# Performance work log

Hardware: AMD Instinct MI355X
Metric: run time of the kernel (lower is better)

Reference implementation:

```python
import jax, jax.numpy as jnp
import numpy as np

N_NODES = 100000
N_EDGES = 1600000
NUM_FEATURES = 128


def setup_inputs() -> dict:
    key = jax.random.key(0)
    ks = jax.random.split(key, 10)
    x = jax.random.normal(ks[0], (N_NODES, NUM_FEATURES), dtype=jnp.float32)
    edge_index = jax.random.randint(ks[1], (2, N_EDGES), 0, N_NODES, dtype=jnp.int64)
    # conv1 MLP: Linear(num_features,128) -> ReLU -> Linear(128,128)
    s1 = 1.0 / np.sqrt(NUM_FEATURES)
    W1 = jax.random.uniform(ks[2], (NUM_FEATURES, 128), jnp.float32, -s1, s1)
    b1 = jax.random.uniform(ks[3], (128,), jnp.float32, -s1, s1)
    s2 = 1.0 / np.sqrt(128)
    W2 = jax.random.uniform(ks[4], (128, 128), jnp.float32, -s2, s2)
    b2 = jax.random.uniform(ks[5], (128,), jnp.float32, -s2, s2)
    # conv2 MLP: Linear(128,64) -> ReLU -> Linear(64,64)
    W3 = jax.random.uniform(ks[6], (128, 64), jnp.float32, -s2, s2)
    b3 = jax.random.uniform(ks[7], (64,), jnp.float32, -s2, s2)
    s3 = 1.0 / np.sqrt(64)
    W4 = jax.random.uniform(ks[8], (64, 64), jnp.float32, -s3, s3)
    b4 = jax.random.uniform(ks[9], (64,), jnp.float32, -s3, s3)
    return {"x": x, "edge_index": edge_index, "W1": W1, "b1": b1,
            "W2": W2, "b2": b2, "W3": W3, "b3": b3, "W4": W4, "b4": b4}


def _gin_conv(x, src, dst, Wa, ba, Wb, bb):
    # GINConv with eps=0: out = MLP(x + sum_{j->i} x_j)
    agg = jax.ops.segment_sum(x[src], dst, num_segments=N_NODES)
    h = x + agg
    h = jax.nn.relu(h @ Wa + ba)
    return h @ Wb + bb


def reference(x, edge_index, W1, b1, W2, b2, W3, b3, W4, b4):
    src, dst = edge_index[0], edge_index[1]
    h = jax.nn.relu(_gin_conv(x, src, dst, W1, b1, W2, b2))
    h = jax.nn.relu(_gin_conv(h, src, dst, W3, b3, W4, b4))
    return h
```

## Files before the change

kernel.cpp:

```cpp
#include <hip/hip_runtime.h>
#include <hip/hip_bf16.h>

#define NODES 100000
#define EDGES 1600000
#define NBINS ((NODES + 127) >> 7)
#define BINCAP 4096
#define PB_BLOCKS 256
#define PB_CHUNK ((EDGES + PB_BLOCKS - 1) / PB_BLOCKS)
#define CAST_BLOCKS 12500
#define WPREP_BLOCKS 176

typedef __bf16 bf16x8 __attribute__((ext_vector_type(8)));
typedef float f32x4 __attribute__((ext_vector_type(4)));

__device__ __forceinline__ unsigned short f2b(float f) {
  __hip_bfloat16 h = __float2bfloat16(f);
  return __builtin_bit_cast(unsigned short, h);
}
__device__ __forceinline__ float b_lo(unsigned u) { return __uint_as_float(u << 16); }
__device__ __forceinline__ float b_hi(unsigned u) { return __uint_as_float(u & 0xffff0000u); }

__global__ __launch_bounds__(256) void prep_count(
    const float4* __restrict__ x4, ushort4* __restrict__ xh4,
    const float* __restrict__ W1, const float* __restrict__ W2,
    const float* __restrict__ W3, const float* __restrict__ W4,
    unsigned short* __restrict__ Wt1, unsigned short* __restrict__ Wt2,
    unsigned short* __restrict__ Wt3, unsigned short* __restrict__ Wt4,
    const int* __restrict__ dst, int* __restrict__ partialT) {
  __shared__ int h[NBINS];
  const int b = blockIdx.x;
  if (b < CAST_BLOCKS) {
    int i = b * 256 + threadIdx.x;
    float4 v = x4[i];
    ushort4 o;
    o.x = f2b(v.x); o.y = f2b(v.y); o.z = f2b(v.z); o.w = f2b(v.w);
    xh4[i] = o;
    return;
  }
  if (b < CAST_BLOCKS + WPREP_BLOCKS) {
    int i = (b - CAST_BLOCKS) * 256 + threadIdx.x;
    if (i < 16384) {
      int n = i >> 7, k = i & 127;
      Wt1[i] = f2b(W1[k * 128 + n]);
    } else if (i < 32768) {
      int j = i - 16384; int n = j >> 7, k = j & 127;
      Wt2[j] = f2b(W2[k * 128 + n]);
    } else if (i < 40960) {
      int j = i - 32768; int n = j >> 7, k = j & 127;
      Wt3[j] = f2b(W3[k * 64 + n]);
    } else if (i < 45056) {
      int j = i - 40960; int n = j >> 6, k = j & 63;
      Wt4[j] = f2b(W4[k * 64 + n]);
    }
    return;
  }
  const int cb = b - CAST_BLOCKS - WPREP_BLOCKS;
  for (int i = threadIdx.x; i < NBINS; i += 256) h[i] = 0;
  __syncthreads();
  const int beg = cb * PB_CHUNK;
  const int end = min(beg + PB_CHUNK, EDGES);
  for (int e = beg + threadIdx.x; e < end; e += 256)
    atomicAdd(&h[dst[e] >> 7], 1);
  __syncthreads();
  for (int i = threadIdx.x; i < NBINS; i += 256)
    partialT[i * PB_BLOCKS + cb] = h[i];
}

__global__ __launch_bounds__(256) void scan_blockoff(const int* __restrict__ partialT,
                                                     int* __restrict__ blockoffT,
                                                     int* __restrict__ binTotal) {
  __shared__ int s[256];
  const int bin = blockIdx.x;
  const int t = threadIdx.x;
  int v = partialT[bin * PB_BLOCKS + t];
  s[t] = v;
  __syncthreads();
  for (int off = 1; off < 256; off <<= 1) {
    int u = (t >= off) ? s[t - off] : 0;
    __syncthreads();
    s[t] += u;
    __syncthreads();
  }
  blockoffT[bin * PB_BLOCKS + t] = s[t] - v;
  if (t == 255) binTotal[bin] = s[255];
}

__global__ __launch_bounds__(1024) void scan_totals(const int* __restrict__ binTotal,
                                                    int* __restrict__ binStart,
                                                    int* __restrict__ rowstart) {
  __shared__ int s[1024];
  const int t = threadIdx.x;
  int v = (t < NBINS) ? binTotal[t] : 0;
  s[t] = v;
  __syncthreads();
  for (int off = 1; off < 1024; off <<= 1) {
    int u = (t >= off) ? s[t - off] : 0;
    __syncthreads();
    s[t] += u;
    __syncthreads();
  }
  if (t < NBINS) binStart[t] = s[t] - v;
  if (t == 0) {
    binStart[NBINS] = EDGES;
    rowstart[NODES] = EDGES;
  }
}

__global__ __launch_bounds__(256) void bin_scatter(const int* __restrict__ src,
                                                   const int* __restrict__ dst,
                                                   const int* __restrict__ binStart,
                                                   const int* __restrict__ blockoffT,
                                                   unsigned* __restrict__ coarse) {
  __shared__ int base[NBINS];
  __shared__ int h[NBINS];
  const int beg = blockIdx.x * PB_CHUNK;
  const int end = min(beg + PB_CHUNK, EDGES);
  for (int i = threadIdx.x; i < NBINS; i += 256) {
    base[i] = binStart[i] + blockoffT[i * PB_BLOCKS + blockIdx.x];
    h[i] = 0;
  }
  __syncthreads();
  for (int e = beg + threadIdx.x; e < end; e += 256) {
    int d = dst[e];
    int b = d >> 7;
    int pos = base[b] + atomicAdd(&h[b], 1);
    coarse[pos] = (unsigned)src[e] | ((unsigned)(d & 127) << 17);
  }
}

__global__ __launch_bounds__(256) void bin_fine(const unsigned* __restrict__ coarse,
                                                const int* __restrict__ binStart,
                                                int* __restrict__ rowstart,
                                                int* __restrict__ bucket) {
  __shared__ unsigned ent[BINCAP];
  __shared__ unsigned obuf[BINCAP];
  __shared__ int deg[128];
  __shared__ int pre[128];
  const int b = blockIdx.x;
  const int t = threadIdx.x;
  const int s0 = binStart[b];
  const int nE = binStart[b + 1] - s0;
  const int binBase = b << 7;

  if (t < 128) deg[t] = 0;
  __syncthreads();
  for (int i = t; i < nE; i += 256) {
    unsigned e = coarse[s0 + i];
    ent[i] = e;
    atomicAdd(&deg[e >> 17], 1);
  }
  __syncthreads();
  int v = 0;
  if (t < 128) {
    v = deg[t];
    pre[t] = v;
  }
  __syncthreads();
  for (int off = 1; off < 128; off <<= 1) {
    int u = (t >= off && t < 128) ? pre[t - off] : 0;
    __syncthreads();
    if (t < 128) pre[t] += u;
    __syncthreads();
  }
  if (t < 128) {
    int ex = pre[t] - v;
    if (binBase + t < NODES) rowstart[binBase + t] = s0 + ex;
    deg[t] = ex;
  }
  __syncthreads();
  for (int i = t; i < nE; i += 256) {
    unsigned e = ent[i];
    int pos = atomicAdd(&deg[e >> 17], 1);
    obuf[pos] = e & 0x1FFFFu;
  }
  __syncthreads();
  for (int i = t; i < nE; i += 256) bucket[s0 + i] = (int)obuf[i];
}

__global__ __launch_bounds__(256) void gather_sum_bf16(
    const uint4* __restrict__ xq, const int* __restrict__ rowstart,
    const int* __restrict__ bucket, uint4* __restrict__ outq) {
  const int n = blockIdx.x * 4 + (threadIdx.x >> 6);
  if (n >= NODES) return;
  const int lane = threadIdx.x & 63;
  const int g = lane >> 4;
  const int fl = lane & 15;

  float a[8] = {0.f, 0.f, 0.f, 0.f, 0.f, 0.f, 0.f, 0.f};
  if (g == 0) {
    uint4 v = xq[(size_t)n * 16 + fl];
    a[0] = b_lo(v.x); a[1] = b_hi(v.x);
    a[2] = b_lo(v.y); a[3] = b_hi(v.y);
    a[4] = b_lo(v.z); a[5] = b_hi(v.z);
    a[6] = b_lo(v.w); a[7] = b_hi(v.w);
  }

  const int beg = rowstart[n];
  const int end = rowstart[n + 1];
  for (int j = beg; j < end; j += 16) {
    int e0 = j + g, e1 = j + 4 + g, e2 = j + 8 + g, e3 = j + 12 + g;
    int i0 = (e0 < end) ? e0 : (end - 1);
    int i1 = (e1 < end) ? e1 : (end - 1);
    int i2 = (e2 < end) ? e2 : (end - 1);
    int i3 = (e3 < end) ? e3 : (end - 1);
    int s0 = bucket[i0], s1 = bucket[i1], s2 = bucket[i2], s3 = bucket[i3];
    uint4 v0 = xq[(size_t)s0 * 16 + fl];
    uint4 v1 = xq[(size_t)s1 * 16 + fl];
    uint4 v2 = xq[(size_t)s2 * 16 + fl];
    uint4 v3 = xq[(size_t)s3 * 16 + fl];
    float m0 = (e0 < end) ? 1.f : 0.f;
    float m1 = (e1 < end) ? 1.f : 0.f;
    float m2 = (e2 < end) ? 1.f : 0.f;
    float m3 = (e3 < end) ? 1.f : 0.f;
    a[0] = fmaf(b_lo(v0.x), m0, a[0]); a[1] = fmaf(b_hi(v0.x), m0, a[1]);
    a[2] = fmaf(b_lo(v0.y), m0, a[2]); a[3] = fmaf(b_hi(v0.y), m0, a[3]);
    a[4] = fmaf(b_lo(v0.z), m0, a[4]); a[5] = fmaf(b_hi(v0.z), m0, a[5]);
    a[6] = fmaf(b_lo(v0.w), m0, a[6]); a[7] = fmaf(b_hi(v0.w), m0, a[7]);
    a[0] = fmaf(b_lo(v1.x), m1, a[0]); a[1] = fmaf(b_hi(v1.x), m1, a[1]);
    a[2] = fmaf(b_lo(v1.y), m1, a[2]); a[3] = fmaf(b_hi(v1.y), m1, a[3]);
    a[4] = fmaf(b_lo(v1.z), m1, a[4]); a[5] = fmaf(b_hi(v1.z), m1, a[5]);
    a[6] = fmaf(b_lo(v1.w), m1, a[6]); a[7] = fmaf(b_hi(v1.w), m1, a[7]);
    a[0] = fmaf(b_lo(v2.x), m2, a[0]); a[1] = fmaf(b_hi(v2.x), m2, a[1]);
    a[2] = fmaf(b_lo(v2.y), m2, a[2]); a[3] = fmaf(b_hi(v2.y), m2, a[3]);
    a[4] = fmaf(b_lo(v2.z), m2, a[4]); a[5] = fmaf(b_hi(v2.z), m2, a[5]);
    a[6] = fmaf(b_lo(v2.w), m2, a[6]); a[7] = fmaf(b_hi(v2.w), m2, a[7]);
    a[0] = fmaf(b_lo(v3.x), m3, a[0]); a[1] = fmaf(b_hi(v3.x), m3, a[1]);
    a[2] = fmaf(b_lo(v3.y), m3, a[2]); a[3] = fmaf(b_hi(v3.y), m3, a[3]);
    a[4] = fmaf(b_lo(v3.z), m3, a[4]); a[5] = fmaf(b_hi(v3.z), m3, a[5]);
    a[6] = fmaf(b_lo(v3.w), m3, a[6]); a[7] = fmaf(b_hi(v3.w), m3, a[7]);
  }

#pragma unroll
  for (int k = 0; k < 8; k++) {
    a[k] += __shfl_xor(a[k], 16, 64);
    a[k] += __shfl_xor(a[k], 32, 64);
  }

  if (lane < 16) {
    uint4 o;
    o.x = ((unsigned)f2b(a[1]) << 16) | f2b(a[0]);
    o.y = ((unsigned)f2b(a[3]) << 16) | f2b(a[2]);
    o.z = ((unsigned)f2b(a[5]) << 16) | f2b(a[4]);
    o.w = ((unsigned)f2b(a[7]) << 16) | f2b(a[6]);
    outq[(size_t)n * 16 + fl] = o;
  }
}

template <int K, int N1, int N2, bool OUT_F32>
__global__ __launch_bounds__(256, 3) void mlp_fused(
    const unsigned short* __restrict__ A,
    const unsigned short* __restrict__ Wa, const float* __restrict__ ba,
    const unsigned short* __restrict__ Wb, const float* __restrict__ bb,
    void* __restrict__ Cout, int M) {
  constexpr int LDA = K + 8;
  constexpr int LWA = K + 8;
  constexpr int LWB = N1 + 8;
  constexpr int NT1 = N1 / 16, KB1 = K / 32;
  constexpr int NT2 = N2 / 16, KB2 = N1 / 32;
  constexpr int WSH = (N1 * LWA > N2 * LWB) ? N1 * LWA : N2 * LWB;
  __shared__ unsigned short S[64 * LDA];
  __shared__ unsigned short Wl[WSH];

  const int tid = threadIdx.x;
  const int wave = tid >> 6;
  const int lane = tid & 63;
  const int g = lane >> 4;
  const int fl = lane & 15;
  const int rowBase = blockIdx.x * 64;

  for (int i = tid; i < 64 * (K / 8); i += 256) {
    int r = i / (K / 8), c = i % (K / 8);
    uint4 v = make_uint4(0, 0, 0, 0);
    if (rowBase + r < M)
      v = ((const uint4*)A)[(size_t)(rowBase + r) * (K / 8) + c];
    *(uint4*)&S[r * LDA + c * 8] = v;
  }
  for (int i = tid; i < N1 * (K / 8); i += 256) {
    int n = i / (K / 8), c = i % (K / 8);
    *(uint4*)&Wl[n * LWA + c * 8] = *(const uint4*)&Wa[(size_t)n * K + c * 8];
  }
  __syncthreads();

  const int arow = wave * 16 + fl;

  f32x4 acc[NT1];
#pragma unroll
  for (int c = 0; c < NT1; c++) acc[c] = (f32x4){0.f, 0.f, 0.f, 0.f};
#pragma unroll
  for (int kb = 0; kb < KB1; kb++) {
    bf16x8 av = *(const bf16x8*)&S[arow * LDA + kb * 32 + g * 8];
#pragma unroll
    for (int c = 0; c < NT1; c++) {
      bf16x8 bv = *(const bf16x8*)&Wl[(c * 16 + fl) * LWA + kb * 32 + g * 8];
      acc[c] = __builtin_amdgcn_mfma_f32_16x16x32_bf16(av, bv, acc[c], 0, 0, 0);
    }
  }

#pragma unroll
  for (int c = 0; c < NT1; c++) {
    int col = c * 16 + fl;
    float bv = ba[col];
#pragma unroll
    for (int reg = 0; reg < 4; reg++) {
      int rloc = wave * 16 + g * 4 + reg;
      S[rloc * LDA + col] = f2b(fmaxf(acc[c][reg] + bv, 0.f));
    }
  }
  __syncthreads();

  for (int i = tid; i < N2 * (N1 / 8); i += 256) {
    int n = i / (N1 / 8), c = i % (N1 / 8);
    *(uint4*)&Wl[n * LWB + c * 8] = *(const uint4*)&Wb[(size_t)n * N1 + c * 8];
  }
  __syncthreads();

  f32x4 acc2[NT2];
#pragma unroll
  for (int c = 0; c < NT2; c++) acc2[c] = (f32x4){0.f, 0.f, 0.f, 0.f};
#pragma unroll
  for (int kb = 0; kb < KB2; kb++) {
    bf16x8 av = *(const bf16x8*)&S[arow * LDA + kb * 32 + g * 8];
#pragma unroll
    for (int c = 0; c < NT2; c++) {
      bf16x8 bv = *(const bf16x8*)&Wl[(c * 16 + fl) * LWB + kb * 32 + g * 8];
      acc2[c] = __builtin_amdgcn_mfma_f32_16x16x32_bf16(av, bv, acc2[c], 0, 0, 0);
    }
  }

#pragma unroll
  for (int c = 0; c < NT2; c++) {
    int col = c * 16 + fl;
    float bv = bb[col];
#pragma unroll
    for (int reg = 0; reg < 4; reg++) {
      int row = rowBase + wave * 16 + g * 4 + reg;
      if (row < M) {
        float v = fmaxf(acc2[c][reg] + bv, 0.f);
        if (OUT_F32)
          ((float*)Cout)[(size_t)row * N2 + col] = v;
        else
          ((unsigned short*)Cout)[(size_t)row * N2 + col] = f2b(v);
      }
    }
  }
}

extern "C" void kernel_launch(void* const* d_in, const int* in_sizes, int n_in,
                              void* d_out, int out_size, void* d_ws, size_t ws_size,
                              hipStream_t stream) {
  const float* x = (const float*)d_in[0];
  const int* ei = (const int*)d_in[1];
  const int* src = ei;
  const int* dst = ei + EDGES;
  const float* W1 = (const float*)d_in[2];
  const float* b1 = (const float*)d_in[3];
  const float* W2 = (const float*)d_in[4];
  const float* b2 = (const float*)d_in[5];
  const float* W3 = (const float*)d_in[6];
  const float* b3 = (const float*)d_in[7];
  const float* W4 = (const float*)d_in[8];
  const float* b4 = (const float*)d_in[9];
  float* out = (float*)d_out;

  char* ws = (char*)d_ws;
  unsigned short* xh = (unsigned short*)ws;
  unsigned short* hA = xh + (size_t)NODES * 128;
  unsigned short* hB = hA + (size_t)NODES * 128;
  unsigned short* Wt1 = hB + (size_t)NODES * 128;
  unsigned short* Wt2 = Wt1 + 128 * 128;
  unsigned short* Wt3 = Wt2 + 128 * 128;
  unsigned short* Wt4 = Wt3 + 64 * 128;
  int* rowstart = (int*)(Wt4 + 64 * 64);
  int* binStart = rowstart + NODES + 1;
  int* binTotal = binStart + NBINS + 1;
  int* partialT = binTotal + NBINS;
  int* blockoffT = partialT + NBINS * PB_BLOCKS;
  unsigned* coarse = (unsigned*)(blockoffT + NBINS * PB_BLOCKS);
  int* bucket = (int*)(coarse + EDGES);

  const int nblocks4 = (NODES + 3) / 4;
  const int gblocks = (NODES + 63) / 64;

  prep_count<<<CAST_BLOCKS + WPREP_BLOCKS + PB_BLOCKS, 256, 0, stream>>>(
      (const float4*)x, (ushort4*)xh, W1, W2, W3, W4, Wt1, Wt2, Wt3, Wt4,
      dst, partialT);
  scan_blockoff<<<NBINS, 256, 0, stream>>>(partialT, blockoffT, binTotal);
  scan_totals<<<1, 1024, 0, stream>>>(binTotal, binStart, rowstart);
  bin_scatter<<<PB_BLOCKS, 256, 0, stream>>>(src, dst, binStart, blockoffT, coarse);
  bin_fine<<<NBINS, 256, 0, stream>>>(coarse, binStart, rowstart, bucket);

  gather_sum_bf16<<<nblocks4, 256, 0, stream>>>((const uint4*)xh, rowstart, bucket,
                                                (uint4*)hA);
  mlp_fused<128, 128, 128, false><<<gblocks, 256, 0, stream>>>(
      hA, Wt1, b1, Wt2, b2, hB, NODES);

  gather_sum_bf16<<<nblocks4, 256, 0, stream>>>((const uint4*)hB, rowstart, bucket,
                                                (uint4*)hA);
  mlp_fused<128, 64, 64, true><<<gblocks, 256, 0, stream>>>(
      hA, Wt3, b3, Wt4, b4, out, NODES);
}
```

Measured before the change: 337.7 us.

## Merge all stages into one persistent cooperative kernel with grid syncs

Replaces the nine separate launches (prep/count, scans, bin scatter, fine binning, two gathers, two MLPs) with a single cooperative persistent kernel that loops over work units and separates phases with grid-wide syncs. The MLP tile now streams weights through a 64-column K-slice buffer so shared memory fits a fixed 35 KB arena and four blocks can reside per CU. This targets launch overhead and inter-kernel gaps. In exchange, each phase is limited to the resident grid size, the MLP reloads weight slices once per tile with extra barriers, and fine binning runs on fewer blocks.

Measured after the change: 937.9 us. 2.78x slower.

```diff
diff --git a/kernel.cpp b/kernel.cpp
--- a/kernel.cpp
+++ b/kernel.cpp
@@ -1,14 +1,17 @@
 #include <hip/hip_runtime.h>
+#include <hip/hip_cooperative_groups.h>
 #include <hip/hip_bf16.h>
+
+namespace cg = cooperative_groups;
 
 #define NODES 100000
 #define EDGES 1600000
 #define NBINS ((NODES + 127) >> 7)
 #define BINCAP 4096
-#define PB_BLOCKS 256
-#define PB_CHUNK ((EDGES + PB_BLOCKS - 1) / PB_BLOCKS)
-#define CAST_BLOCKS 12500
-#define WPREP_BLOCKS 176
+#define GMAX 1024
+#define NTILES ((NODES + 63) / 64)
+#define NQUADS ((NODES + 3) / 4)
+#define SMEM_BYTES 35840
 
 typedef __bf16 bf16x8 __attribute__((ext_vector_type(8)));
 typedef float f32x4 __attribute__((ext_vector_type(4)));
@@ -20,169 +23,25 @@
 __device__ __forceinline__ float b_lo(unsigned u) { return __uint_as_float(u << 16); }
 __device__ __forceinline__ float b_hi(unsigned u) { return __uint_as_float(u & 0xffff0000u); }
 
-__global__ __launch_bounds__(256) void prep_count(
-    const float4* __restrict__ x4, ushort4* __restrict__ xh4,
-    const float* __restrict__ W1, const float* __restrict__ W2,
-    const float* __restrict__ W3, const float* __restrict__ W4,
-    unsigned short* __restrict__ Wt1, unsigned short* __restrict__ Wt2,
-    unsigned short* __restrict__ Wt3, unsigned short* __restrict__ Wt4,
-    const int* __restrict__ dst, int* __restrict__ partialT) {
-  __shared__ int h[NBINS];
-  const int b = blockIdx.x;
-  if (b < CAST_BLOCKS) {
-    int i = b * 256 + threadIdx.x;
-    float4 v = x4[i];
-    ushort4 o;
-    o.x = f2b(v.x); o.y = f2b(v.y); o.z = f2b(v.z); o.w = f2b(v.w);
-    xh4[i] = o;
-    return;
-  }
-  if (b < CAST_BLOCKS + WPREP_BLOCKS) {
-    int i = (b - CAST_BLOCKS) * 256 + threadIdx.x;
-    if (i < 16384) {
-      int n = i >> 7, k = i & 127;
-      Wt1[i] = f2b(W1[k * 128 + n]);
-    } else if (i < 32768) {
-      int j = i - 16384; int n = j >> 7, k = j & 127;
-      Wt2[j] = f2b(W2[k * 128 + n]);
-    } else if (i < 40960) {
-      int j = i - 32768; int n = j >> 7, k = j & 127;
-      Wt3[j] = f2b(W3[k * 64 + n]);
-    } else if (i < 45056) {
-      int j = i - 40960; int n = j >> 6, k = j & 63;
-      Wt4[j] = f2b(W4[k * 64 + n]);
-    }
-    return;
-  }
-  const int cb = b - CAST_BLOCKS - WPREP_BLOCKS;
-  for (int i = threadIdx.x; i < NBINS; i += 256) h[i] = 0;
-  __syncthreads();
-  const int beg = cb * PB_CHUNK;
-  const int end = min(beg + PB_CHUNK, EDGES);
-  for (int e = beg + threadIdx.x; e < end; e += 256)
-    atomicAdd(&h[dst[e] >> 7], 1);
-  __syncthreads();
-  for (int i = threadIdx.x; i < NBINS; i += 256)
-    partialT[i * PB_BLOCKS + cb] = h[i];
-}
-
-__global__ __launch_bounds__(256) void scan_blockoff(const int* __restrict__ partialT,
-                                                     int* __restrict__ blockoffT,
-                                                     int* __restrict__ binTotal) {
-  __shared__ int s[256];
-  const int bin = blockIdx.x;
-  const int t = threadIdx.x;
-  int v = partialT[bin * PB_BLOCKS + t];
-  s[t] = v;
-  __syncthreads();
-  for (int off = 1; off < 256; off <<= 1) {
-    int u = (t >= off) ? s[t - off] : 0;
-    __syncthreads();
-    s[t] += u;
-    __syncthreads();
-  }
-  blockoffT[bin * PB_BLOCKS + t] = s[t] - v;
-  if (t == 255) binTotal[bin] = s[255];
-}
-
-__global__ __launch_bounds__(1024) void scan_totals(const int* __restrict__ binTotal,
-                                                    int* __restrict__ binStart,
-                                                    int* __restrict__ rowstart) {
-  __shared__ int s[1024];
-  const int t = threadIdx.x;
-  int v = (t < NBINS) ? binTotal[t] : 0;
-  s[t] = v;
-  __syncthreads();
-  for (int off = 1; off < 1024; off <<= 1) {
-    int u = (t >= off) ? s[t - off] : 0;
-    __syncthreads();
-    s[t] += u;
-    __syncthreads();
-  }
-  if (t < NBINS) binStart[t] = s[t] - v;
-  if (t == 0) {
-    binStart[NBINS] = EDGES;
-    rowstart[NODES] = EDGES;
-  }
-}
-
-__global__ __launch_bounds__(256) void bin_scatter(const int* __restrict__ src,
-                                                   const int* __restrict__ dst,
-                                                   const int* __restrict__ binStart,
-                                                   const int* __restrict__ blockoffT,
-                                                   unsigned* __restrict__ coarse) {
-  __shared__ int base[NBINS];
-  __shared__ int h[NBINS];
-  const int beg = blockIdx.x * PB_CHUNK;
-  const int end = min(beg + PB_CHUNK, EDGES);
-  for (int i = threadIdx.x; i < NBINS; i += 256) {
-    base[i] = binStart[i] + blockoffT[i * PB_BLOCKS + blockIdx.x];
-    h[i] = 0;
-  }
-  __syncthreads();
-  for (int e = beg + threadIdx.x; e < end; e += 256) {
-    int d = dst[e];
-    int b = d >> 7;
-    int pos = base[b] + atomicAdd(&h[b], 1);
-    coarse[pos] = (unsigned)src[e] | ((unsigned)(d & 127) << 17);
-  }
-}
-
-__global__ __launch_bounds__(256) void bin_fine(const unsigned* __restrict__ coarse,
-                                                const int* __restrict__ binStart,
-                                                int* __restrict__ rowstart,
-                                                int* __restrict__ bucket) {
-  __shared__ unsigned ent[BINCAP];
-  __shared__ unsigned obuf[BINCAP];
-  __shared__ int deg[128];
-  __shared__ int pre[128];
-  const int b = blockIdx.x;
-  const int t = threadIdx.x;
-  const int s0 = binStart[b];
-  const int nE = binStart[b + 1] - s0;
-  const int binBase = b << 7;
-
-  if (t < 128) deg[t] = 0;
-  __syncthreads();
-  for (int i = t; i < nE; i += 256) {
-    unsigned e = coarse[s0 + i];
-    ent[i] = e;
-    atomicAdd(&deg[e >> 17], 1);
-  }
-  __syncthreads();
-  int v = 0;
-  if (t < 128) {
-    v = deg[t];
-    pre[t] = v;
-  }
-  __syncthreads();
-  for (int off = 1; off < 128; off <<= 1) {
-    int u = (t >= off && t < 128) ? pre[t - off] : 0;
-    __syncthreads();
-    if (t < 128) pre[t] += u;
-    __syncthreads();
-  }
-  if (t < 128) {
-    int ex = pre[t] - v;
-    if (binBase + t < NODES) rowstart[binBase + t] = s0 + ex;
-    deg[t] = ex;
-  }
-  __syncthreads();
-  for (int i = t; i < nE; i += 256) {
-    unsigned e = ent[i];
-    int pos = atomicAdd(&deg[e >> 17], 1);
-    obuf[pos] = e & 0x1FFFFu;
-  }
-  __syncthreads();
-  for (int i = t; i < nE; i += 256) bucket[s0 + i] = (int)obuf[i];
-}
-
-__global__ __launch_bounds__(256) void gather_sum_bf16(
+struct MegaParams {
+  const float4* x4;
+  const int* src;
+  const int* dst;
+  const float* W1; const float* b1; const float* W2; const float* b2;
+  const float* W3; const float* b3; const float* W4; const float* b4;
+  unsigned short* xh; unsigned short* hA; unsigned short* hB;
+  unsigned short* Wt1; unsigned short* Wt2; unsigned short* Wt3; unsigned short* Wt4;
+  int* rowstart; int* binStart; int* binTotal; int* partialT; int* blockoffT;
+  unsigned* coarse; int* bucket;
+  float* out;
+};
+
+__device__ __forceinline__ void gather_quad(
     const uint4* __restrict__ xq, const int* __restrict__ rowstart,
-    const int* __restrict__ bucket, uint4* __restrict__ outq) {
-  const int n = blockIdx.x * 4 + (threadIdx.x >> 6);
+    const int* __restrict__ bucket, uint4* __restrict__ outq, int u, int tid) {
+  const int n = u * 4 + (tid >> 6);
   if (n >= NODES) return;
-  const int lane = threadIdx.x & 63;
+  const int lane = tid & 63;
   const int g = lane >> 4;
   const int fl = lane & 15;
 
@@ -194,7 +53,6 @@
     a[4] = b_lo(v.z); a[5] = b_hi(v.z);
     a[6] = b_lo(v.w); a[7] = b_hi(v.w);
   }
-
   const int beg = rowstart[n];
   const int end = rowstart[n + 1];
   for (int j = beg; j < end; j += 16) {
@@ -229,13 +87,11 @@
     a[4] = fmaf(b_lo(v3.z), m3, a[4]); a[5] = fmaf(b_hi(v3.z), m3, a[5]);
     a[6] = fmaf(b_lo(v3.w), m3, a[6]); a[7] = fmaf(b_hi(v3.w), m3, a[7]);
   }
-
 #pragma unroll
   for (int k = 0; k < 8; k++) {
     a[k] += __shfl_xor(a[k], 16, 64);
     a[k] += __shfl_xor(a[k], 32, 64);
   }
-
   if (lane < 16) {
     uint4 o;
     o.x = ((unsigned)f2b(a[1]) << 16) | f2b(a[0]);
@@ -247,55 +103,51 @@
 }
 
 template <int K, int N1, int N2, bool OUT_F32>
-__global__ __launch_bounds__(256, 3) void mlp_fused(
+__device__ __forceinline__ void mlp_tile(
     const unsigned short* __restrict__ A,
     const unsigned short* __restrict__ Wa, const float* __restrict__ ba,
     const unsigned short* __restrict__ Wb, const float* __restrict__ bb,
-    void* __restrict__ Cout, int M) {
+    void* __restrict__ Cout, int tile, int tid, char* smem) {
   constexpr int LDA = K + 8;
-  constexpr int LWA = K + 8;
-  constexpr int LWB = N1 + 8;
-  constexpr int NT1 = N1 / 16, KB1 = K / 32;
-  constexpr int NT2 = N2 / 16, KB2 = N1 / 32;
-  constexpr int WSH = (N1 * LWA > N2 * LWB) ? N1 * LWA : N2 * LWB;
-  __shared__ unsigned short S[64 * LDA];
-  __shared__ unsigned short Wl[WSH];
-
-  const int tid = threadIdx.x;
-  const int wave = tid >> 6;
-  const int lane = tid & 63;
-  const int g = lane >> 4;
-  const int fl = lane & 15;
-  const int rowBase = blockIdx.x * 64;
+  constexpr int LWS = 72;
+  constexpr int NT1 = N1 / 16, NT2 = N2 / 16;
+  constexpr int NSL1 = K / 64, NSL2 = N1 / 64;
+  unsigned short* S = (unsigned short*)smem;
+  unsigned short* Wbuf = S + 64 * LDA;
+
+  const int wave = tid >> 6, lane = tid & 63, g = lane >> 4, fl = lane & 15;
+  const int rowBase = tile * 64;
+  const int arow = wave * 16 + fl;
 
   for (int i = tid; i < 64 * (K / 8); i += 256) {
     int r = i / (K / 8), c = i % (K / 8);
     uint4 v = make_uint4(0, 0, 0, 0);
-    if (rowBase + r < M)
+    if (rowBase + r < NODES)
       v = ((const uint4*)A)[(size_t)(rowBase + r) * (K / 8) + c];
     *(uint4*)&S[r * LDA + c * 8] = v;
   }
-  for (int i = tid; i < N1 * (K / 8); i += 256) {
-    int n = i / (K / 8), c = i % (K / 8);
-    *(uint4*)&Wl[n * LWA + c * 8] = *(const uint4*)&Wa[(size_t)n * K + c * 8];
-  }
-  __syncthreads();
-
-  const int arow = wave * 16 + fl;
 
   f32x4 acc[NT1];
 #pragma unroll
   for (int c = 0; c < NT1; c++) acc[c] = (f32x4){0.f, 0.f, 0.f, 0.f};
 #pragma unroll
-  for (int kb = 0; kb < KB1; kb++) {
-    bf16x8 av = *(const bf16x8*)&S[arow * LDA + kb * 32 + g * 8];
-#pragma unroll
-    for (int c = 0; c < NT1; c++) {
-      bf16x8 bv = *(const bf16x8*)&Wl[(c * 16 + fl) * LWA + kb * 32 + g * 8];
-      acc[c] = __builtin_amdgcn_mfma_f32_16x16x32_bf16(av, bv, acc[c], 0, 0, 0);
-    }
-  }
-
+  for (int s = 0; s < NSL1; s++) {
+    for (int i = tid; i < N1 * 8; i += 256) {
+      int n = i >> 3, c = i & 7;
+      *(uint4*)&Wbuf[n * LWS + c * 8] = *(const uint4*)&Wa[(size_t)n * K + s * 64 + c * 8];
+    }
+    __syncthreads();
+#pragma unroll
+    for (int kbl = 0; kbl < 2; kbl++) {
+      bf16x8 av = *(const bf16x8*)&S[arow * LDA + (s * 2 + kbl) * 32 + g * 8];
+#pragma unroll
+      for (int c = 0; c < NT1; c++) {
+        bf16x8 bv = *(const bf16x8*)&Wbuf[(c * 16 + fl) * LWS + kbl * 32 + g * 8];
+        acc[c] = __builtin_amdgcn_mfma_f32_16x16x32_bf16(av, bv, acc[c], 0, 0, 0);
+      }
+    }
+    __syncthreads();
+  }
 #pragma unroll
   for (int c = 0; c < NT1; c++) {
     int col = c * 16 + fl;
@@ -306,27 +158,27 @@
       S[rloc * LDA + col] = f2b(fmaxf(acc[c][reg] + bv, 0.f));
     }
   }
-  __syncthreads();
-
-  for (int i = tid; i < N2 * (N1 / 8); i += 256) {
-    int n = i / (N1 / 8), c = i % (N1 / 8);
-    *(uint4*)&Wl[n * LWB + c * 8] = *(const uint4*)&Wb[(size_t)n * N1 + c * 8];
-  }
-  __syncthreads();
-
   f32x4 acc2[NT2];
 #pragma unroll
   for (int c = 0; c < NT2; c++) acc2[c] = (f32x4){0.f, 0.f, 0.f, 0.f};
 #pragma unroll
-  for (int kb = 0; kb < KB2; kb++) {
-    bf16x8 av = *(const bf16x8*)&S[arow * LDA + kb * 32 + g * 8];
-#pragma unroll
-    for (int c = 0; c < NT2; c++) {
-      bf16x8 bv = *(const bf16x8*)&Wl[(c * 16 + fl) * LWB + kb * 32 + g * 8];
-      acc2[c] = __builtin_amdgcn_mfma_f32_16x16x32_bf16(av, bv, acc2[c], 0, 0, 0);
-    }
-  }
-
+  for (int s = 0; s < NSL2; s++) {
+    for (int i = tid; i < N2 * 8; i += 256) {
+      int n = i >> 3, c = i & 7;
+      *(uint4*)&Wbuf[n * LWS + c * 8] = *(const uint4*)&Wb[(size_t)n * N1 + s * 64 + c * 8];
+    }
+    __syncthreads();
+#pragma unroll
+    for (int kbl = 0; kbl < 2; kbl++) {
+      bf16x8 av = *(const bf16x8*)&S[arow * LDA + (s * 2 + kbl) * 32 + g * 8];
+#pragma unroll
+      for (int c = 0; c < NT2; c++) {
+        bf16x8 bv = *(const bf16x8*)&Wbuf[(c * 16 + fl) * LWS + kbl * 32 + g * 8];
+        acc2[c] = __builtin_amdgcn_mfma_f32_16x16x32_bf16(av, bv, acc2[c], 0, 0, 0);
+      }
+    }
+    __syncthreads();
+  }
 #pragma unroll
   for (int c = 0; c < NT2; c++) {
     int col = c * 16 + fl;
@@ -334,7 +186,7 @@
 #pragma unroll
     for (int reg = 0; reg < 4; reg++) {
       int row = rowBase + wave * 16 + g * 4 + reg;
-      if (row < M) {
+      if (row < NODES) {
         float v = fmaxf(acc2[c][reg] + bv, 0.f);
         if (OUT_F32)
           ((float*)Cout)[(size_t)row * N2 + col] = v;
@@ -345,57 +197,209 @@
   }
 }
 
+__global__ __launch_bounds__(256, 4) void gin_mega(MegaParams p) {
+  __shared__ __align__(16) char smem[SMEM_BYTES];
+  cg::grid_group gg = cg::this_grid();
+  const int tid = threadIdx.x;
+  const int bid = blockIdx.x;
+  const int gd = gridDim.x;
+
+  {
+    const size_t stride = (size_t)gd * 256;
+    for (size_t i = (size_t)bid * 256 + tid; i < (size_t)NODES * 32; i += stride) {
+      float4 v = p.x4[i];
+      ushort4 o;
+      o.x = f2b(v.x); o.y = f2b(v.y); o.z = f2b(v.z); o.w = f2b(v.w);
+      ((ushort4*)p.xh)[i] = o;
+    }
+    for (int i = bid * 256 + tid; i < 45056; i += gd * 256) {
+      if (i < 16384) { int n = i >> 7, k = i & 127; p.Wt1[i] = f2b(p.W1[k * 128 + n]); }
+      else if (i < 32768) { int j = i - 16384; int n = j >> 7, k = j & 127; p.Wt2[j] = f2b(p.W2[k * 128 + n]); }
+      else if (i < 40960) { int j = i - 32768; int n = j >> 7, k = j & 127; p.Wt3[j] = f2b(p.W3[k * 64 + n]); }
+      else { int j = i - 40960; int n = j >> 6, k = j & 63; p.Wt4[j] = f2b(p.W4[k * 64 + n]); }
+    }
+    int* h = (int*)smem;
+    for (int i = tid; i < NBINS; i += 256) h[i] = 0;
+    __syncthreads();
+    const int chunk = (EDGES + gd - 1) / gd;
+    const int beg = bid * chunk, end = min(beg + chunk, EDGES);
+    for (int e = beg + tid; e < end; e += 256) atomicAdd(&h[p.dst[e] >> 7], 1);
+    __syncthreads();
+    for (int i = tid; i < NBINS; i += 256) p.partialT[(size_t)i * GMAX + bid] = h[i];
+  }
+  gg.sync();
+
+  for (int bin = bid; bin < NBINS; bin += gd) {
+    int* s = (int*)smem;
+    const size_t base = (size_t)bin * GMAX;
+    int v[4]; int sum = 0;
+#pragma unroll
+    for (int k = 0; k < 4; k++) {
+      int idx = tid * 4 + k;
+      v[k] = (idx < gd) ? p.partialT[base + idx] : 0;
+      sum += v[k];
+    }
+    s[tid] = sum;
+    __syncthreads();
+    for (int off = 1; off < 256; off <<= 1) {
+      int u = (tid >= off) ? s[tid - off] : 0;
+      __syncthreads();
+      s[tid] += u;
+      __syncthreads();
+    }
+    int run = s[tid] - sum;
+#pragma unroll
+    for (int k = 0; k < 4; k++) {
+      int idx = tid * 4 + k;
+      if (idx < gd) p.blockoffT[base + idx] = run;
+      run += v[k];
+    }
+    if (tid == 255) p.binTotal[bin] = s[255];
+    __syncthreads();
+  }
+  gg.sync();
+
+  if (bid == 0) {
+    int* s = (int*)smem;
+    int v[4]; int sum = 0;
+#pragma unroll
+    for (int k = 0; k < 4; k++) {
+      int idx = tid * 4 + k;
+      v[k] = (idx < NBINS) ? p.binTotal[idx] : 0;
+      sum += v[k];
+    }
+    s[tid] = sum;
+    __syncthreads();
+    for (int off = 1; off < 256; off <<= 1) {
+      int u = (tid >= off) ? s[tid - off] : 0;
+      __syncthreads();
+      s[tid] += u;
+      __syncthreads();
+    }
+    int run = s[tid] - sum;
+#pragma unroll
+    for (int k = 0; k < 4; k++) {
+      int idx = tid * 4 + k;
+      if (idx < NBINS) p.binStart[idx] = run;
+      run += v[k];
+    }
+    if (tid == 0) { p.binStart[NBINS] = EDGES; p.rowstart[NODES] = EDGES; }
+  }
+  gg.sync();
+
+  {
+    int* base = (int*)smem;
+    int* h = base + NBINS;
+    for (int i = tid; i < NBINS; i += 256) {
+      base[i] = p.binStart[i] + p.blockoffT[(size_t)i * GMAX + bid];
+      h[i] = 0;
+    }
+    __syncthreads();
+    const int chunk = (EDGES + gd - 1) / gd;
+    const int beg = bid * chunk, end = min(beg + chunk, EDGES);
+    for (int e = beg + tid; e < end; e += 256) {
+      int d = p.dst[e];
+      int b = d >> 7;
+      int pos = base[b] + atomicAdd(&h[b], 1);
+      p.coarse[pos] = (unsigned)p.src[e] | ((unsigned)(d & 127) << 17);
+    }
+  }
+  gg.sync();
+
+  for (int b = bid; b < NBINS; b += gd) {
+    unsigned* ent = (unsigned*)smem;
+    unsigned* obuf = ent + BINCAP;
+    int* deg = (int*)(obuf + BINCAP);
+    int* pre = deg + 128;
+    const int s0 = p.binStart[b];
+    const int nE = p.binStart[b + 1] - s0;
+    const int binBase = b << 7;
+    if (tid < 128) deg[tid] = 0;
+    __syncthreads();
+    for (int i = tid; i < nE; i += 256) {
+      unsigned e = p.coarse[s0 + i];
+      ent[i] = e;
+      atomicAdd(&deg[e >> 17], 1);
+    }
+    __syncthreads();
+    int v = 0;
+    if (tid < 128) { v = deg[tid]; pre[tid] = v; }
+    __syncthreads();
+    for (int off = 1; off < 128; off <<= 1) {
+      int u = (tid >= off && tid < 128) ? pre[tid - off] : 0;
+      __syncthreads();
+      if (tid < 128) pre[tid] += u;
+      __syncthreads();
+    }
+    if (tid < 128) {
+      int ex = pre[tid] - v;
+      if (binBase + tid < NODES) p.rowstart[binBase + tid] = s0 + ex;
+      deg[tid] = ex;
+    }
+    __syncthreads();
+    for (int i = tid; i < nE; i += 256) {
+      unsigned e = ent[i];
+      int pos = atomicAdd(&deg[e >> 17], 1);
+      obuf[pos] = e & 0x1FFFFu;
+    }
+    __syncthreads();
+    for (int i = tid; i < nE; i += 256) p.bucket[s0 + i] = (int)obuf[i];
+    __syncthreads();
+  }
+  gg.sync();
+
+  for (int u = bid; u < NQUADS; u += gd)
+    gather_quad((const uint4*)p.xh, p.rowstart, p.bucket, (uint4*)p.hA, u, tid);
+  gg.sync();
+
+  for (int t = bid; t < NTILES; t += gd)
+    mlp_tile<128, 128, 128, false>(p.hA, p.Wt1, p.b1, p.Wt2, p.b2, p.hB, t, tid, smem);
+  gg.sync();
+
+  for (int u = bid; u < NQUADS; u += gd)
+    gather_quad((const uint4*)p.hB, p.rowstart, p.bucket, (uint4*)p.hA, u, tid);
+  gg.sync();
+
+  for (int t = bid; t < NTILES; t += gd)
+    mlp_tile<128, 64, 64, true>(p.hA, p.Wt3, p.b3, p.Wt4, p.b4, p.out, t, tid, smem);
+}
+
 extern "C" void kernel_launch(void* const* d_in, const int* in_sizes, int n_in,
                               void* d_out, int out_size, void* d_ws, size_t ws_size,
                               hipStream_t stream) {
-  const float* x = (const float*)d_in[0];
+  MegaParams p;
+  p.x4 = (const float4*)d_in[0];
   const int* ei = (const int*)d_in[1];
-  const int* src = ei;
-  const int* dst = ei + EDGES;
-  const float* W1 = (const float*)d_in[2];
-  const float* b1 = (const float*)d_in[3];
-  const float* W2 = (const float*)d_in[4];
-  const float* b2 = (const float*)d_in[5];
-  const float* W3 = (const float*)d_in[6];
-  const float* b3 = (const float*)d_in[7];
-  const float* W4 = (const float*)d_in[8];
-  const float* b4 = (const float*)d_in[9];
-  float* out = (float*)d_out;
+  p.src = ei;
+  p.dst = ei + EDGES;
+  p.W1 = (const float*)d_in[2];  p.b1 = (const float*)d_in[3];
+  p.W2 = (const float*)d_in[4];  p.b2 = (const float*)d_in[5];
+  p.W3 = (const float*)d_in[6];  p.b3 = (const float*)d_in[7];
+  p.W4 = (const float*)d_in[8];  p.b4 = (const float*)d_in[9];
+  p.out = (float*)d_out;
 
   char* ws = (char*)d_ws;
-  unsigned short* xh = (unsigned short*)ws;
-  unsigned short* hA = xh + (size_t)NODES * 128;
-  unsigned short* hB = hA + (size_t)NODES * 128;
-  unsigned short* Wt1 = hB + (size_t)NODES * 128;
-  unsigned short* Wt2 = Wt1 + 128 * 128;
-  unsigned short* Wt3 = Wt2 + 128 * 128;
-  unsigned short* Wt4 = Wt3 + 64 * 128;
-  int* rowstart = (int*)(Wt4 + 64 * 64);
-  int* binStart = rowstart + NODES + 1;
-  int* binTotal = binStart + NBINS + 1;
-  int* partialT = binTotal + NBINS;
-  int* blockoffT = partialT + NBINS * PB_BLOCKS;
-  unsigned* coarse = (unsigned*)(blockoffT + NBINS * PB_BLOCKS);
-  int* bucket = (int*)(coarse + EDGES);
-
-  const int nblocks4 = (NODES + 3) / 4;
-  const int gblocks = (NODES + 63) / 64;
-
-  prep_count<<<CAST_BLOCKS + WPREP_BLOCKS + PB_BLOCKS, 256, 0, stream>>>(
-      (const float4*)x, (ushort4*)xh, W1, W2, W3, W4, Wt1, Wt2, Wt3, Wt4,
-      dst, partialT);
-  scan_blockoff<<<NBINS, 256, 0, stream>>>(partialT, blockoffT, binTotal);
-  scan_totals<<<1, 1024, 0, stream>>>(binTotal, binStart, rowstart);
-  bin_scatter<<<PB_BLOCKS, 256, 0, stream>>>(src, dst, binStart, blockoffT, coarse);
-  bin_fine<<<NBINS, 256, 0, stream>>>(coarse, binStart, rowstart, bucket);
-
-  gather_sum_bf16<<<nblocks4, 256, 0, stream>>>((const uint4*)xh, rowstart, bucket,
-                                                (uint4*)hA);
-  mlp_fused<128, 128, 128, false><<<gblocks, 256, 0, stream>>>(
-      hA, Wt1, b1, Wt2, b2, hB, NODES);
-
-  gather_sum_bf16<<<nblocks4, 256, 0, stream>>>((const uint4*)hB, rowstart, bucket,
-                                                (uint4*)hA);
-  mlp_fused<128, 64, 64, true><<<gblocks, 256, 0, stream>>>(
-      hA, Wt3, b3, Wt4, b4, out, NODES);
+  p.xh = (unsigned short*)ws;
+  p.hA = p.xh + (size_t)NODES * 128;
+  p.hB = p.hA + (size_t)NODES * 128;
+  p.Wt1 = p.hB + (size_t)NODES * 128;
+  p.Wt2 = p.Wt1 + 128 * 128;
+  p.Wt3 = p.Wt2 + 128 * 128;
+  p.Wt4 = p.Wt3 + 64 * 128;
+  p.rowstart = (int*)(p.Wt4 + 64 * 64);
+  p.binStart = p.rowstart + NODES + 1;
+  p.binTotal = p.binStart + NBINS + 1;
+  p.partialT = p.binTotal + NBINS;
+  p.blockoffT = p.partialT + (size_t)NBINS * GMAX;
+  p.coarse = (unsigned*)(p.blockoffT + (size_t)NBINS * GMAX);
+  p.bucket = (int*)(p.coarse + EDGES);
+
+  int maxb = 0;
+  hipOccupancyMaxActiveBlocksPerMultiprocessor(&maxb, gin_mega, 256, 0);
+  int grid = maxb * 256;
+  if (grid > GMAX) grid = GMAX;
+  if (grid < 256) grid = 256;
+
+  void* args[] = {(void*)&p};
+  hipLaunchCooperativeKernel(gin_mega, dim3(grid), dim3(256), args, 0, stream);
 }
```
